# Performance work log

Measured on AMD Instinct MI355X. Metric: run time of the kernel, lower is better.

Reference implementation:

```python
import jax, jax.numpy as jnp
import numpy as np

BATCH = 16
N_ROIS = 1000
NUM_CLASSES = 81
DET_MAX = 100
MIN_CONF = 0.7
NMS_THRESH = 0.3
BBOX_STD = jnp.array([0.1, 0.1, 0.2, 0.2], jnp.float32)


def setup_inputs() -> dict:
    key = jax.random.key(0)
    k1, k2, k3, k4, k5 = jax.random.split(key, 5)
    # valid normalized boxes (y1,x1,y2,x2) with y2>y1, x2>x1
    y1 = jax.random.uniform(k1, (BATCH, N_ROIS, 1)) * 0.7
    x1 = jax.random.uniform(k2, (BATCH, N_ROIS, 1)) * 0.7
    hw = jax.random.uniform(k3, (BATCH, N_ROIS, 2)) * 0.28 + 0.02
    rois = jnp.concatenate([y1, x1, y1 + hw[..., :1], x1 + hw[..., 1:]], axis=-1)
    fpn_class = jax.nn.softmax(jax.random.normal(k4, (BATCH, N_ROIS, NUM_CLASSES)) * 2.0, axis=-1)
    fpn_bbox = jax.random.normal(k5, (BATCH, N_ROIS, NUM_CLASSES, 4)) * 0.1
    window = jnp.tile(jnp.array([[0.0, 0.0, 1.0, 1.0]], jnp.float32), (BATCH, 1))
    return {"rois": rois, "fpn_class": fpn_class, "fpn_bbox": fpn_bbox, "window": window}


def apply_box_deltas(boxes, deltas):
    # boxes [N,4] (y1,x1,y2,x2), deltas [N,4] (dy,dx,log dh,log dw)
    h = boxes[:, 2] - boxes[:, 0]
    w = boxes[:, 3] - boxes[:, 1]
    cy = boxes[:, 0] + 0.5 * h
    cx = boxes[:, 1] + 0.5 * w
    cy = cy + deltas[:, 0] * h
    cx = cx + deltas[:, 1] * w
    h = h * jnp.exp(deltas[:, 2])
    w = w * jnp.exp(deltas[:, 3])
    y1 = cy - 0.5 * h
    x1 = cx - 0.5 * w
    return jnp.stack([y1, x1, y1 + h, x1 + w], axis=1)


def clip_boxes(boxes, window):
    wy1, wx1, wy2, wx2 = window[0], window[1], window[2], window[3]
    y1 = jnp.clip(boxes[:, 0], wy1, wy2)
    x1 = jnp.clip(boxes[:, 1], wx1, wx2)
    y2 = jnp.clip(boxes[:, 2], wy1, wy2)
    x2 = jnp.clip(boxes[:, 3], wx1, wx2)
    return jnp.stack([y1, x1, y2, x2], axis=1)


def box_iou(a, b):
    # a [N,4], b [M,4] -> [N,M]
    y1 = jnp.maximum(a[:, None, 0], b[None, :, 0])
    x1 = jnp.maximum(a[:, None, 1], b[None, :, 1])
    y2 = jnp.minimum(a[:, None, 2], b[None, :, 2])
    x2 = jnp.minimum(a[:, None, 3], b[None, :, 3])
    inter = jnp.maximum(y2 - y1, 0.0) * jnp.maximum(x2 - x1, 0.0)
    area_a = (a[:, 2] - a[:, 0]) * (a[:, 3] - a[:, 1])
    area_b = (b[:, 2] - b[:, 0]) * (b[:, 3] - b[:, 1])
    union = area_a[:, None] + area_b[None, :] - inter
    return inter / jnp.maximum(union, 1e-10)


def per_class_nms_mask(boxes, class_ids, scores):
    """boxes [N,4], class_ids [N] int, scores [N] (already -1 where pre-filtered).
    Returns bool [N]: survives greedy per-class NMS (max DET_MAX kept per class)."""
    fg = jnp.arange(1, NUM_CLASSES)                       # [C-1] skip background
    sc = jnp.where(class_ids[None, :] == fg[:, None], scores[None, :], -1.0)  # [C-1,N]
    order = jnp.argsort(-sc, axis=1)                      # [C-1,N] score-desc per class
    iou = box_iou(boxes, boxes)                           # [N,N]
    col = jnp.arange(N_ROIS)
    active0 = sc >= 0.0
    kept0 = jnp.zeros_like(active0)
    cnt0 = jnp.zeros((NUM_CLASSES - 1,), jnp.int32)

    def body(i, carry):
        active, kept, cnt = carry
        cur = order[:, i]                                  # [C-1] current box idx per class
        is_act = jnp.take_along_axis(active, cur[:, None], axis=1)[:, 0]
        is_kept = is_act & (cnt < DET_MAX)
        cnt = cnt + is_kept.astype(jnp.int32)
        kept = kept | ((col[None, :] == cur[:, None]) & is_kept[:, None])
        suppress = is_kept[:, None] & (iou[cur] > NMS_THRESH)  # [C-1,N]
        active = active & ~suppress
        return (active, kept, cnt)

    _, kept, _ = jax.lax.fori_loop(0, N_ROIS, body, (active0, kept0, cnt0))
    return kept.any(axis=0)


def _refine_one(rois, probs, deltas, window):
    n = jnp.arange(N_ROIS)
    class_ids = jnp.argmax(probs, axis=1)                 # [N]
    class_scores = probs[n, class_ids]                    # [N]
    d = deltas[n, class_ids] * BBOX_STD                   # [N,4]
    refined = clip_boxes(apply_box_deltas(rois, d), window)
    keep = (class_ids > 0) & (class_scores >= MIN_CONF)
    sg = jax.lax.stop_gradient
    nms_keep = per_class_nms_mask(
        sg(refined), class_ids, jnp.where(keep, sg(class_scores), -1.0))
    keep = keep & nms_keep
    sf = jnp.where(keep, class_scores, -1.0)
    top_s, top_i = jax.lax.top_k(sf, DET_MAX)             # keep top DET_MAX overall
    valid = top_s >= 0.0
    det = jnp.concatenate(
        [refined[top_i],
         class_ids[top_i][:, None].astype(jnp.float32),
         class_scores[top_i][:, None]], axis=1)           # [DET_MAX,6]
    return jnp.where(valid[:, None], det, 0.0)            # zero-pad invalid rows


def reference(rois, fpn_class, fpn_bbox, window):
    # [B, DET_MAX, 6] = (y1,x1,y2,x2,class_id,score), normalized coords
    return jax.vmap(_refine_one)(rois, fpn_class, fpn_bbox, window)
```

## Files before the change

### kernel.cpp

```cpp
#include <hip/hip_runtime.h>
#include <math.h>

#define BATCH 16
#define N_ROIS 1000
#define NUM_CLASSES 81
#define DET_MAX 100
#define MIN_CONF 0.7f
#define NMS_THRESH 0.3f

#define ROI_TILE 128

__global__ __launch_bounds__(256) void refine_v4(
    const float* __restrict__ rois, const float* __restrict__ probs,
    const float* __restrict__ deltas, const float* __restrict__ window,
    float* __restrict__ ws_box, float* __restrict__ ws_score, int* __restrict__ ws_cls)
{
    __shared__ float s_probs[ROI_TILE * NUM_CLASSES];

    const int base_roi = blockIdx.x * ROI_TILE;

    const float4* src = (const float4*)(probs + (size_t)base_roi * NUM_CLASSES);
    float4* dst = (float4*)s_probs;
    for (int i = threadIdx.x; i < ROI_TILE * NUM_CLASSES / 4; i += 256)
        dst[i] = src[i];
    __syncthreads();

    if (threadIdx.x < ROI_TILE) {
        const int idx = base_roi + threadIdx.x;
        const int b = idx / N_ROIS;

        const float* p = s_probs + threadIdx.x * NUM_CLASSES;
        float bs0 = p[0], bs1 = p[1], bs2 = p[2], bs3 = p[3];
        int ib0 = 0, ib1 = 1, ib2 = 2, ib3 = 3;
        #pragma unroll
        for (int c = 4; c <= 76; c += 4) {
            float v0 = p[c], v1 = p[c + 1], v2 = p[c + 2], v3 = p[c + 3];
            if (v0 > bs0) { bs0 = v0; ib0 = c; }
            if (v1 > bs1) { bs1 = v1; ib1 = c + 1; }
            if (v2 > bs2) { bs2 = v2; ib2 = c + 2; }
            if (v3 > bs3) { bs3 = v3; ib3 = c + 3; }
        }
        { float v = p[80]; if (v > bs0) { bs0 = v; ib0 = 80; } }
        if (bs1 > bs0 || (bs1 == bs0 && ib1 < ib0)) { bs0 = bs1; ib0 = ib1; }
        if (bs3 > bs2 || (bs3 == bs2 && ib3 < ib2)) { bs2 = bs3; ib2 = ib3; }
        if (bs2 > bs0 || (bs2 == bs0 && ib2 < ib0)) { bs0 = bs2; ib0 = ib2; }
        const float bs = bs0;
        const int best = ib0;

        const bool keep = (best > 0) && (bs >= MIN_CONF);
        ws_score[idx] = keep ? bs : -1.0f;

        if (keep) {
            const float4 dd = ((const float4*)deltas)[(size_t)idx * NUM_CLASSES + best];
            float dy = dd.x * 0.1f, dx = dd.y * 0.1f, dh = dd.z * 0.2f, dw = dd.w * 0.2f;

            const float4 rr = ((const float4*)rois)[idx];
            float y1 = rr.x, x1 = rr.y, y2 = rr.z, x2 = rr.w;
            float h = y2 - y1, w = x2 - x1;
            float cy = y1 + 0.5f * h, cx = x1 + 0.5f * w;
            cy += dy * h;
            cx += dx * w;
            h *= expf(dh);
            w *= expf(dw);
            float ny1 = cy - 0.5f * h;
            float nx1 = cx - 0.5f * w;
            float ny2 = ny1 + h;
            float nx2 = nx1 + w;

            const float* win = window + b * 4;
            float wy1 = win[0], wx1 = win[1], wy2 = win[2], wx2 = win[3];
            ny1 = fminf(fmaxf(ny1, wy1), wy2);
            nx1 = fminf(fmaxf(nx1, wx1), wx2);
            ny2 = fminf(fmaxf(ny2, wy1), wy2);
            nx2 = fminf(fmaxf(nx2, wx1), wx2);

            ((float4*)ws_box)[idx] = make_float4(ny1, nx1, ny2, nx2);
            ws_cls[idx] = best;
        }
    }
}

__global__ __launch_bounds__(256) void nms_v4(
    const float* __restrict__ ws_box, const float* __restrict__ ws_score,
    const int* __restrict__ ws_cls, float* __restrict__ out)
{
    const int b = blockIdx.x;
    const int tid = threadIdx.x;

    __shared__ float s_cbox[N_ROIS][4];
    __shared__ float s_csc[N_ROIS];
    __shared__ short s_cidx[N_ROIS];
    __shared__ unsigned char s_ccls[N_ROIS];
    __shared__ float s_sbox[N_ROIS][4];
    __shared__ float s_ssc[N_ROIS];
    __shared__ unsigned char s_scls[N_ROIS];
    __shared__ unsigned char s_kept[N_ROIS];
    __shared__ short s_bucket[N_ROIS];
    __shared__ int s_cnt[NUM_CLASSES];
    __shared__ int s_off[NUM_CLASSES];
    __shared__ int s_C;

    if (tid == 0) s_C = 0;
    if (tid < NUM_CLASSES) s_cnt[tid] = 0;

    for (int i = tid; i < DET_MAX * 6; i += 256)
        out[(size_t)b * DET_MAX * 6 + i] = 0.0f;
    __syncthreads();

    for (int i = tid; i < N_ROIS; i += 256) {
        float sc = ws_score[b * N_ROIS + i];
        if (sc >= 0.0f) {
            int k = atomicAdd(&s_C, 1);
            s_csc[k] = sc;
            s_cidx[k] = (short)i;
            int c = ws_cls[b * N_ROIS + i];
            s_ccls[k] = (unsigned char)c;
            atomicAdd(&s_cnt[c], 1);
            float4 bb = ((const float4*)ws_box)[b * N_ROIS + i];
            s_cbox[k][0] = bb.x; s_cbox[k][1] = bb.y;
            s_cbox[k][2] = bb.z; s_cbox[k][3] = bb.w;
        }
    }
    __syncthreads();
    const int C = s_C;

    if (tid == 0) {
        int acc = 0;
        for (int c = 0; c < NUM_CLASSES; ++c) { s_off[c] = acc; acc += s_cnt[c]; }
    }
    __syncthreads();

    for (int k = tid; k < C; k += 256) {
        float sk = s_csc[k];
        int ik = s_cidx[k];
        int ck = s_ccls[k];
        int rank = 0, crank = 0;
        for (int j = 0; j < C; ++j) {
            float sj = s_csc[j];
            int before = (sj > sk) | ((sj == sk) & (s_cidx[j] < ik));
            rank += before;
            crank += before & (s_ccls[j] == ck);
        }
        s_ssc[rank] = sk;
        s_scls[rank] = (unsigned char)ck;
        s_sbox[rank][0] = s_cbox[k][0];
        s_sbox[rank][1] = s_cbox[k][1];
        s_sbox[rank][2] = s_cbox[k][2];
        s_sbox[rank][3] = s_cbox[k][3];
        s_kept[rank] = 0;
        s_bucket[s_off[ck] + crank] = (short)rank;
    }
    __syncthreads();

    if (tid >= 1 && tid < NUM_CLASSES) {
        const int off = s_off[tid];
        const int m = s_cnt[tid];
        int kept_cnt = 0;
        for (int a = 0; a < m; ++a) {
            if (kept_cnt >= DET_MAX) break;
            int i = s_bucket[off + a];
            float b0 = s_sbox[i][0], b1 = s_sbox[i][1];
            float b2 = s_sbox[i][2], b3 = s_sbox[i][3];
            float area_b = (b2 - b0) * (b3 - b1);
            bool sup = false;
            for (int q = 0; q < a; ++q) {
                int j = s_bucket[off + q];
                if (!s_kept[j]) continue;
                float a0 = s_sbox[j][0], a1 = s_sbox[j][1];
                float a2 = s_sbox[j][2], a3 = s_sbox[j][3];
                float yy1 = fmaxf(a0, b0);
                float xx1 = fmaxf(a1, b1);
                float yy2 = fminf(a2, b2);
                float xx2 = fminf(a3, b3);
                float inter = fmaxf(yy2 - yy1, 0.0f) * fmaxf(xx2 - xx1, 0.0f);
                float area_a = (a2 - a0) * (a3 - a1);
                float uni = area_a + area_b - inter;
                if (inter / fmaxf(uni, 1e-10f) > NMS_THRESH) { sup = true; break; }
            }
            if (!sup) { s_kept[i] = 1; ++kept_cnt; }
        }
    }
    __syncthreads();

    for (int i = tid; i < C; i += 256) {
        if (s_kept[i]) {
            int slot = 0;
            for (int j = 0; j < i; ++j) slot += s_kept[j];
            if (slot < DET_MAX) {
                float* o = out + (size_t)b * DET_MAX * 6 + slot * 6;
                o[0] = s_sbox[i][0];
                o[1] = s_sbox[i][1];
                o[2] = s_sbox[i][2];
                o[3] = s_sbox[i][3];
                o[4] = (float)s_scls[i];
                o[5] = s_ssc[i];
            }
        }
    }
}

extern "C" void kernel_launch(void* const* d_in, const int* in_sizes, int n_in,
                              void* d_out, int out_size, void* d_ws, size_t ws_size,
                              hipStream_t stream) {
    const float* rois      = (const float*)d_in[0];
    const float* fpn_class = (const float*)d_in[1];
    const float* fpn_bbox  = (const float*)d_in[2];
    const float* window    = (const float*)d_in[3];
    float* out = (float*)d_out;

    float* ws_box   = (float*)d_ws;
    float* ws_score = ws_box + (size_t)BATCH * N_ROIS * 4;
    int*   ws_cls   = (int*)(ws_score + (size_t)BATCH * N_ROIS);

    refine_v4<<<BATCH * N_ROIS / ROI_TILE, 256, 0, stream>>>(
        rois, fpn_class, fpn_bbox, window, ws_box, ws_score, ws_cls);
    nms_v4<<<BATCH, 256, 0, stream>>>(ws_box, ws_score, ws_cls, out);
}
```

Baseline: 85.03 us.

## Fuse refine and NMS into one per-image kernel with aliased shared memory

Merges the ROI refinement kernel into the NMS kernel so each block processes one image, tiling class probabilities through shared memory and appending kept candidates directly to shared arrays. This removes a kernel launch and the global workspace write/read between stages. Shared buffers for probs and sorted boxes are aliased, and box accesses are vectorized to float4. The refine phase now runs on only 16 blocks, which reduces parallelism for the probability scan.

```diff
diff --git a/kernel.cpp b/kernel.cpp
--- a/kernel.cpp
+++ b/kernel.cpp
@@ -8,94 +8,28 @@
 #define MIN_CONF 0.7f
 #define NMS_THRESH 0.3f
 
-#define ROI_TILE 128
+#define TILE 256
 
-__global__ __launch_bounds__(256) void refine_v4(
+__global__ __launch_bounds__(256) void detect_fused_v5(
     const float* __restrict__ rois, const float* __restrict__ probs,
     const float* __restrict__ deltas, const float* __restrict__ window,
-    float* __restrict__ ws_box, float* __restrict__ ws_score, int* __restrict__ ws_cls)
-{
-    __shared__ float s_probs[ROI_TILE * NUM_CLASSES];
-
-    const int base_roi = blockIdx.x * ROI_TILE;
-
-    const float4* src = (const float4*)(probs + (size_t)base_roi * NUM_CLASSES);
-    float4* dst = (float4*)s_probs;
-    for (int i = threadIdx.x; i < ROI_TILE * NUM_CLASSES / 4; i += 256)
-        dst[i] = src[i];
-    __syncthreads();
-
-    if (threadIdx.x < ROI_TILE) {
-        const int idx = base_roi + threadIdx.x;
-        const int b = idx / N_ROIS;
-
-        const float* p = s_probs + threadIdx.x * NUM_CLASSES;
-        float bs0 = p[0], bs1 = p[1], bs2 = p[2], bs3 = p[3];
-        int ib0 = 0, ib1 = 1, ib2 = 2, ib3 = 3;
-        #pragma unroll
-        for (int c = 4; c <= 76; c += 4) {
-            float v0 = p[c], v1 = p[c + 1], v2 = p[c + 2], v3 = p[c + 3];
-            if (v0 > bs0) { bs0 = v0; ib0 = c; }
-            if (v1 > bs1) { bs1 = v1; ib1 = c + 1; }
-            if (v2 > bs2) { bs2 = v2; ib2 = c + 2; }
-            if (v3 > bs3) { bs3 = v3; ib3 = c + 3; }
-        }
-        { float v = p[80]; if (v > bs0) { bs0 = v; ib0 = 80; } }
-        if (bs1 > bs0 || (bs1 == bs0 && ib1 < ib0)) { bs0 = bs1; ib0 = ib1; }
-        if (bs3 > bs2 || (bs3 == bs2 && ib3 < ib2)) { bs2 = bs3; ib2 = ib3; }
-        if (bs2 > bs0 || (bs2 == bs0 && ib2 < ib0)) { bs0 = bs2; ib0 = ib2; }
-        const float bs = bs0;
-        const int best = ib0;
-
-        const bool keep = (best > 0) && (bs >= MIN_CONF);
-        ws_score[idx] = keep ? bs : -1.0f;
-
-        if (keep) {
-            const float4 dd = ((const float4*)deltas)[(size_t)idx * NUM_CLASSES + best];
-            float dy = dd.x * 0.1f, dx = dd.y * 0.1f, dh = dd.z * 0.2f, dw = dd.w * 0.2f;
-
-            const float4 rr = ((const float4*)rois)[idx];
-            float y1 = rr.x, x1 = rr.y, y2 = rr.z, x2 = rr.w;
-            float h = y2 - y1, w = x2 - x1;
-            float cy = y1 + 0.5f * h, cx = x1 + 0.5f * w;
-            cy += dy * h;
-            cx += dx * w;
-            h *= expf(dh);
-            w *= expf(dw);
-            float ny1 = cy - 0.5f * h;
-            float nx1 = cx - 0.5f * w;
-            float ny2 = ny1 + h;
-            float nx2 = nx1 + w;
-
-            const float* win = window + b * 4;
-            float wy1 = win[0], wx1 = win[1], wy2 = win[2], wx2 = win[3];
-            ny1 = fminf(fmaxf(ny1, wy1), wy2);
-            nx1 = fminf(fmaxf(nx1, wx1), wx2);
-            ny2 = fminf(fmaxf(ny2, wy1), wy2);
-            nx2 = fminf(fmaxf(nx2, wx1), wx2);
-
-            ((float4*)ws_box)[idx] = make_float4(ny1, nx1, ny2, nx2);
-            ws_cls[idx] = best;
-        }
-    }
-}
-
-__global__ __launch_bounds__(256) void nms_v4(
-    const float* __restrict__ ws_box, const float* __restrict__ ws_score,
-    const int* __restrict__ ws_cls, float* __restrict__ out)
+    float* __restrict__ out)
 {
     const int b = blockIdx.x;
     const int tid = threadIdx.x;
 
-    __shared__ float s_cbox[N_ROIS][4];
+    __shared__ __align__(16) char s_raw[TILE * NUM_CLASSES * 4];
+    float* const s_probs = (float*)s_raw;
+    float (*const s_sbox)[4]    = (float(*)[4])s_raw;
+    float* const s_ssc          = (float*)(s_raw + 16000);
+    unsigned char* const s_scls = (unsigned char*)(s_raw + 20000);
+    unsigned char* const s_kept = (unsigned char*)(s_raw + 21000);
+    short* const s_bucket       = (short*)(s_raw + 22000);
+
+    __shared__ __align__(16) float s_cbox[N_ROIS][4];
     __shared__ float s_csc[N_ROIS];
     __shared__ short s_cidx[N_ROIS];
     __shared__ unsigned char s_ccls[N_ROIS];
-    __shared__ float s_sbox[N_ROIS][4];
-    __shared__ float s_ssc[N_ROIS];
-    __shared__ unsigned char s_scls[N_ROIS];
-    __shared__ unsigned char s_kept[N_ROIS];
-    __shared__ short s_bucket[N_ROIS];
     __shared__ int s_cnt[NUM_CLASSES];
     __shared__ int s_off[NUM_CLASSES];
     __shared__ int s_C;
@@ -105,23 +39,72 @@
 
     for (int i = tid; i < DET_MAX * 6; i += 256)
         out[(size_t)b * DET_MAX * 6 + i] = 0.0f;
+
+    const float4 wv = ((const float4*)window)[b];
     __syncthreads();
 
-    for (int i = tid; i < N_ROIS; i += 256) {
-        float sc = ws_score[b * N_ROIS + i];
-        if (sc >= 0.0f) {
-            int k = atomicAdd(&s_C, 1);
-            s_csc[k] = sc;
-            s_cidx[k] = (short)i;
-            int c = ws_cls[b * N_ROIS + i];
-            s_ccls[k] = (unsigned char)c;
-            atomicAdd(&s_cnt[c], 1);
-            float4 bb = ((const float4*)ws_box)[b * N_ROIS + i];
-            s_cbox[k][0] = bb.x; s_cbox[k][1] = bb.y;
-            s_cbox[k][2] = bb.z; s_cbox[k][3] = bb.w;
+    for (int t0 = 0; t0 < N_ROIS; t0 += TILE) {
+        const int tn = (N_ROIS - t0 < TILE) ? (N_ROIS - t0) : TILE;
+
+        const float4* src = (const float4*)(probs + ((size_t)b * N_ROIS + t0) * NUM_CLASSES);
+        const int n4 = tn * NUM_CLASSES / 4;
+        for (int i = tid; i < n4; i += 256)
+            ((float4*)s_probs)[i] = src[i];
+        __syncthreads();
+
+        if (tid < tn) {
+            const int r = t0 + tid;
+            const float* p = s_probs + tid * NUM_CLASSES;
+            float bs0 = p[0], bs1 = p[1], bs2 = p[2], bs3 = p[3];
+            int ib0 = 0, ib1 = 1, ib2 = 2, ib3 = 3;
+            #pragma unroll
+            for (int c = 4; c <= 76; c += 4) {
+                float v0 = p[c], v1 = p[c + 1], v2 = p[c + 2], v3 = p[c + 3];
+                if (v0 > bs0) { bs0 = v0; ib0 = c; }
+                if (v1 > bs1) { bs1 = v1; ib1 = c + 1; }
+                if (v2 > bs2) { bs2 = v2; ib2 = c + 2; }
+                if (v3 > bs3) { bs3 = v3; ib3 = c + 3; }
+            }
+            { float v = p[80]; if (v > bs0) { bs0 = v; ib0 = 80; } }
+            if (bs1 > bs0 || (bs1 == bs0 && ib1 < ib0)) { bs0 = bs1; ib0 = ib1; }
+            if (bs3 > bs2 || (bs3 == bs2 && ib3 < ib2)) { bs2 = bs3; ib2 = ib3; }
+            if (bs2 > bs0 || (bs2 == bs0 && ib2 < ib0)) { bs0 = bs2; ib0 = ib2; }
+            const float bs = bs0;
+            const int best = ib0;
+
+            if ((best > 0) && (bs >= MIN_CONF)) {
+                const size_t gidx = (size_t)b * N_ROIS + r;
+                const float4 dd = ((const float4*)deltas)[gidx * NUM_CLASSES + best];
+                float dy = dd.x * 0.1f, dx = dd.y * 0.1f, dh = dd.z * 0.2f, dw = dd.w * 0.2f;
+
+                const float4 rr = ((const float4*)rois)[gidx];
+                float y1 = rr.x, x1 = rr.y, y2 = rr.z, x2 = rr.w;
+                float h = y2 - y1, w = x2 - x1;
+                float cy = y1 + 0.5f * h, cx = x1 + 0.5f * w;
+                cy += dy * h;
+                cx += dx * w;
+                h *= expf(dh);
+                w *= expf(dw);
+                float ny1 = cy - 0.5f * h;
+                float nx1 = cx - 0.5f * w;
+                float ny2 = ny1 + h;
+                float nx2 = nx1 + w;
+
+                ny1 = fminf(fmaxf(ny1, wv.x), wv.z);
+                nx1 = fminf(fmaxf(nx1, wv.y), wv.w);
+                ny2 = fminf(fmaxf(ny2, wv.x), wv.z);
+                nx2 = fminf(fmaxf(nx2, wv.y), wv.w);
+
+                const int k = atomicAdd(&s_C, 1);
+                s_csc[k] = bs;
+                s_cidx[k] = (short)r;
+                s_ccls[k] = (unsigned char)best;
+                atomicAdd(&s_cnt[best], 1);
+                ((float4*)s_cbox)[k] = make_float4(ny1, nx1, ny2, nx2);
+            }
         }
+        __syncthreads();
     }
-    __syncthreads();
     const int C = s_C;
 
     if (tid == 0) {
@@ -143,10 +126,7 @@
         }
         s_ssc[rank] = sk;
         s_scls[rank] = (unsigned char)ck;
-        s_sbox[rank][0] = s_cbox[k][0];
-        s_sbox[rank][1] = s_cbox[k][1];
-        s_sbox[rank][2] = s_cbox[k][2];
-        s_sbox[rank][3] = s_cbox[k][3];
+        ((float4*)s_sbox)[rank] = ((const float4*)s_cbox)[k];
         s_kept[rank] = 0;
         s_bucket[s_off[ck] + crank] = (short)rank;
     }
@@ -159,21 +139,19 @@
         for (int a = 0; a < m; ++a) {
             if (kept_cnt >= DET_MAX) break;
             int i = s_bucket[off + a];
-            float b0 = s_sbox[i][0], b1 = s_sbox[i][1];
-            float b2 = s_sbox[i][2], b3 = s_sbox[i][3];
-            float area_b = (b2 - b0) * (b3 - b1);
+            float4 bb = ((const float4*)s_sbox)[i];
+            float area_b = (bb.z - bb.x) * (bb.w - bb.y);
             bool sup = false;
             for (int q = 0; q < a; ++q) {
                 int j = s_bucket[off + q];
                 if (!s_kept[j]) continue;
-                float a0 = s_sbox[j][0], a1 = s_sbox[j][1];
-                float a2 = s_sbox[j][2], a3 = s_sbox[j][3];
-                float yy1 = fmaxf(a0, b0);
-                float xx1 = fmaxf(a1, b1);
-                float yy2 = fminf(a2, b2);
-                float xx2 = fminf(a3, b3);
+                float4 aa = ((const float4*)s_sbox)[j];
+                float yy1 = fmaxf(aa.x, bb.x);
+                float xx1 = fmaxf(aa.y, bb.y);
+                float yy2 = fminf(aa.z, bb.z);
+                float xx2 = fminf(aa.w, bb.w);
                 float inter = fmaxf(yy2 - yy1, 0.0f) * fmaxf(xx2 - xx1, 0.0f);
-                float area_a = (a2 - a0) * (a3 - a1);
+                float area_a = (aa.z - aa.x) * (aa.w - aa.y);
                 float uni = area_a + area_b - inter;
                 if (inter / fmaxf(uni, 1e-10f) > NMS_THRESH) { sup = true; break; }
             }
@@ -188,10 +166,11 @@
             for (int j = 0; j < i; ++j) slot += s_kept[j];
             if (slot < DET_MAX) {
                 float* o = out + (size_t)b * DET_MAX * 6 + slot * 6;
-                o[0] = s_sbox[i][0];
-                o[1] = s_sbox[i][1];
-                o[2] = s_sbox[i][2];
-                o[3] = s_sbox[i][3];
+                float4 bb = ((const float4*)s_sbox)[i];
+                o[0] = bb.x;
+                o[1] = bb.y;
+                o[2] = bb.z;
+                o[3] = bb.w;
                 o[4] = (float)s_scls[i];
                 o[5] = s_ssc[i];
             }
@@ -207,12 +186,7 @@
     const float* fpn_bbox  = (const float*)d_in[2];
     const float* window    = (const float*)d_in[3];
     float* out = (float*)d_out;
+    (void)d_ws; (void)ws_size;
 
-    float* ws_box   = (float*)d_ws;
-    float* ws_score = ws_box + (size_t)BATCH * N_ROIS * 4;
-    int*   ws_cls   = (int*)(ws_score + (size_t)BATCH * N_ROIS);
-
-    refine_v4<<<BATCH * N_ROIS / ROI_TILE, 256, 0, stream>>>(
-        rois, fpn_class, fpn_bbox, window, ws_box, ws_score, ws_cls);
-    nms_v4<<<BATCH, 256, 0, stream>>>(ws_box, ws_score, ws_cls, out);
+    detect_fused_v5<<<BATCH, 256, 0, stream>>>(rois, fpn_class, fpn_bbox, window, out);
 }
```

Result: slower. 111.2 us (+30.8%).

## Fuse refine and NMS into one cooperative kernel with grid sync

Applied to the files above, without the earlier changes.

Merges the refine kernel and the per-batch NMS kernel into a single cooperative launch, using a grid-wide sync in place of the kernel boundary and a shared-memory arena reused by both phases. This targets the second launch's overhead and the gap between kernels. Box accesses in shared memory are also changed to float4 loads and stores. In exchange it adds a cooperative-launch and grid-barrier cost, and the larger shared footprint may limit how many blocks fit per CU.

```diff
diff --git a/kernel.cpp b/kernel.cpp
--- a/kernel.cpp
+++ b/kernel.cpp
@@ -1,5 +1,8 @@
 #include <hip/hip_runtime.h>
+#include <hip/hip_cooperative_groups.h>
 #include <math.h>
+
+namespace cg = cooperative_groups;
 
 #define BATCH 16
 #define N_ROIS 1000
@@ -9,96 +12,101 @@
 #define NMS_THRESH 0.3f
 
 #define ROI_TILE 128
-
-__global__ __launch_bounds__(256) void refine_v4(
+#define GRID_BLOCKS (BATCH * N_ROIS / ROI_TILE)
+
+__global__ __launch_bounds__(256) void detect_coop_v6(
     const float* __restrict__ rois, const float* __restrict__ probs,
     const float* __restrict__ deltas, const float* __restrict__ window,
-    float* __restrict__ ws_box, float* __restrict__ ws_score, int* __restrict__ ws_cls)
+    float* __restrict__ ws_box, float* __restrict__ ws_score,
+    int* __restrict__ ws_cls, float* __restrict__ out)
 {
-    __shared__ float s_probs[ROI_TILE * NUM_CLASSES];
-
-    const int base_roi = blockIdx.x * ROI_TILE;
-
-    const float4* src = (const float4*)(probs + (size_t)base_roi * NUM_CLASSES);
-    float4* dst = (float4*)s_probs;
-    for (int i = threadIdx.x; i < ROI_TILE * NUM_CLASSES / 4; i += 256)
-        dst[i] = src[i];
-    __syncthreads();
-
-    if (threadIdx.x < ROI_TILE) {
-        const int idx = base_roi + threadIdx.x;
-        const int b = idx / N_ROIS;
-
-        const float* p = s_probs + threadIdx.x * NUM_CLASSES;
-        float bs0 = p[0], bs1 = p[1], bs2 = p[2], bs3 = p[3];
-        int ib0 = 0, ib1 = 1, ib2 = 2, ib3 = 3;
-        #pragma unroll
-        for (int c = 4; c <= 76; c += 4) {
-            float v0 = p[c], v1 = p[c + 1], v2 = p[c + 2], v3 = p[c + 3];
-            if (v0 > bs0) { bs0 = v0; ib0 = c; }
-            if (v1 > bs1) { bs1 = v1; ib1 = c + 1; }
-            if (v2 > bs2) { bs2 = v2; ib2 = c + 2; }
-            if (v3 > bs3) { bs3 = v3; ib3 = c + 3; }
-        }
-        { float v = p[80]; if (v > bs0) { bs0 = v; ib0 = 80; } }
-        if (bs1 > bs0 || (bs1 == bs0 && ib1 < ib0)) { bs0 = bs1; ib0 = ib1; }
-        if (bs3 > bs2 || (bs3 == bs2 && ib3 < ib2)) { bs2 = bs3; ib2 = ib3; }
-        if (bs2 > bs0 || (bs2 == bs0 && ib2 < ib0)) { bs0 = bs2; ib0 = ib2; }
-        const float bs = bs0;
-        const int best = ib0;
-
-        const bool keep = (best > 0) && (bs >= MIN_CONF);
-        ws_score[idx] = keep ? bs : -1.0f;
-
-        if (keep) {
-            const float4 dd = ((const float4*)deltas)[(size_t)idx * NUM_CLASSES + best];
-            float dy = dd.x * 0.1f, dx = dd.y * 0.1f, dh = dd.z * 0.2f, dw = dd.w * 0.2f;
-
-            const float4 rr = ((const float4*)rois)[idx];
-            float y1 = rr.x, x1 = rr.y, y2 = rr.z, x2 = rr.w;
-            float h = y2 - y1, w = x2 - x1;
-            float cy = y1 + 0.5f * h, cx = x1 + 0.5f * w;
-            cy += dy * h;
-            cx += dx * w;
-            h *= expf(dh);
-            w *= expf(dw);
-            float ny1 = cy - 0.5f * h;
-            float nx1 = cx - 0.5f * w;
-            float ny2 = ny1 + h;
-            float nx2 = nx1 + w;
-
-            const float* win = window + b * 4;
-            float wy1 = win[0], wx1 = win[1], wy2 = win[2], wx2 = win[3];
-            ny1 = fminf(fmaxf(ny1, wy1), wy2);
-            nx1 = fminf(fmaxf(nx1, wx1), wx2);
-            ny2 = fminf(fmaxf(ny2, wy1), wy2);
-            nx2 = fminf(fmaxf(nx2, wx1), wx2);
-
-            ((float4*)ws_box)[idx] = make_float4(ny1, nx1, ny2, nx2);
-            ws_cls[idx] = best;
-        }
-    }
-}
-
-__global__ __launch_bounds__(256) void nms_v4(
-    const float* __restrict__ ws_box, const float* __restrict__ ws_score,
-    const int* __restrict__ ws_cls, float* __restrict__ out)
-{
-    const int b = blockIdx.x;
-    const int tid = threadIdx.x;
-
-    __shared__ float s_cbox[N_ROIS][4];
-    __shared__ float s_csc[N_ROIS];
-    __shared__ short s_cidx[N_ROIS];
-    __shared__ unsigned char s_ccls[N_ROIS];
-    __shared__ float s_sbox[N_ROIS][4];
-    __shared__ float s_ssc[N_ROIS];
-    __shared__ unsigned char s_scls[N_ROIS];
-    __shared__ unsigned char s_kept[N_ROIS];
-    __shared__ short s_bucket[N_ROIS];
+    __shared__ __align__(16) char arena[47680];
+    __shared__ int s_C;
     __shared__ int s_cnt[NUM_CLASSES];
     __shared__ int s_off[NUM_CLASSES];
-    __shared__ int s_C;
+
+    const int tid = threadIdx.x;
+
+    {
+        float* s_probs = (float*)arena;
+        const int base_roi = blockIdx.x * ROI_TILE;
+
+        const float4* src = (const float4*)(probs + (size_t)base_roi * NUM_CLASSES);
+        float4* dst = (float4*)s_probs;
+        for (int i = tid; i < ROI_TILE * NUM_CLASSES / 4; i += 256)
+            dst[i] = src[i];
+        __syncthreads();
+
+        if (tid < ROI_TILE) {
+            const int idx = base_roi + tid;
+            const int b = idx / N_ROIS;
+
+            const float* p = s_probs + tid * NUM_CLASSES;
+            float bs0 = p[0], bs1 = p[1], bs2 = p[2], bs3 = p[3];
+            int ib0 = 0, ib1 = 1, ib2 = 2, ib3 = 3;
+            #pragma unroll
+            for (int c = 4; c <= 76; c += 4) {
+                float v0 = p[c], v1 = p[c + 1], v2 = p[c + 2], v3 = p[c + 3];
+                if (v0 > bs0) { bs0 = v0; ib0 = c; }
+                if (v1 > bs1) { bs1 = v1; ib1 = c + 1; }
+                if (v2 > bs2) { bs2 = v2; ib2 = c + 2; }
+                if (v3 > bs3) { bs3 = v3; ib3 = c + 3; }
+            }
+            { float v = p[80]; if (v > bs0) { bs0 = v; ib0 = 80; } }
+            if (bs1 > bs0 || (bs1 == bs0 && ib1 < ib0)) { bs0 = bs1; ib0 = ib1; }
+            if (bs3 > bs2 || (bs3 == bs2 && ib3 < ib2)) { bs2 = bs3; ib2 = ib3; }
+            if (bs2 > bs0 || (bs2 == bs0 && ib2 < ib0)) { bs0 = bs2; ib0 = ib2; }
+            const float bs = bs0;
+            const int best = ib0;
+
+            const bool keep = (best > 0) && (bs >= MIN_CONF);
+            ws_score[idx] = keep ? bs : -1.0f;
+
+            if (keep) {
+                const float4 dd = ((const float4*)deltas)[(size_t)idx * NUM_CLASSES + best];
+                float dy = dd.x * 0.1f, dx = dd.y * 0.1f, dh = dd.z * 0.2f, dw = dd.w * 0.2f;
+
+                const float4 rr = ((const float4*)rois)[idx];
+                float y1 = rr.x, x1 = rr.y, y2 = rr.z, x2 = rr.w;
+                float h = y2 - y1, w = x2 - x1;
+                float cy = y1 + 0.5f * h, cx = x1 + 0.5f * w;
+                cy += dy * h;
+                cx += dx * w;
+                h *= expf(dh);
+                w *= expf(dw);
+                float ny1 = cy - 0.5f * h;
+                float nx1 = cx - 0.5f * w;
+                float ny2 = ny1 + h;
+                float nx2 = nx1 + w;
+
+                const float* win = window + b * 4;
+                float wy1 = win[0], wx1 = win[1], wy2 = win[2], wx2 = win[3];
+                ny1 = fminf(fmaxf(ny1, wy1), wy2);
+                nx1 = fminf(fmaxf(nx1, wx1), wx2);
+                ny2 = fminf(fmaxf(ny2, wy1), wy2);
+                nx2 = fminf(fmaxf(nx2, wx1), wx2);
+
+                ((float4*)ws_box)[idx] = make_float4(ny1, nx1, ny2, nx2);
+                ws_cls[idx] = best;
+            }
+        }
+    }
+
+    __threadfence();
+    cg::this_grid().sync();
+
+    if (blockIdx.x >= BATCH) return;
+    const int b = blockIdx.x;
+
+    float (*const s_cbox)[4]    = (float(*)[4])(arena);
+    float (*const s_sbox)[4]    = (float(*)[4])(arena + 16000);
+    float* const s_csc          = (float*)(arena + 32000);
+    float* const s_ssc          = (float*)(arena + 36000);
+    short* const s_cidx         = (short*)(arena + 40000);
+    short* const s_bucket       = (short*)(arena + 42000);
+    unsigned char* const s_ccls = (unsigned char*)(arena + 44000);
+    unsigned char* const s_scls = (unsigned char*)(arena + 45000);
+    unsigned char* const s_kept = (unsigned char*)(arena + 46000);
 
     if (tid == 0) s_C = 0;
     if (tid < NUM_CLASSES) s_cnt[tid] = 0;
@@ -117,8 +125,7 @@
             s_ccls[k] = (unsigned char)c;
             atomicAdd(&s_cnt[c], 1);
             float4 bb = ((const float4*)ws_box)[b * N_ROIS + i];
-            s_cbox[k][0] = bb.x; s_cbox[k][1] = bb.y;
-            s_cbox[k][2] = bb.z; s_cbox[k][3] = bb.w;
+            ((float4*)s_cbox)[k] = bb;
         }
     }
     __syncthreads();
@@ -143,10 +150,7 @@
         }
         s_ssc[rank] = sk;
         s_scls[rank] = (unsigned char)ck;
-        s_sbox[rank][0] = s_cbox[k][0];
-        s_sbox[rank][1] = s_cbox[k][1];
-        s_sbox[rank][2] = s_cbox[k][2];
-        s_sbox[rank][3] = s_cbox[k][3];
+        ((float4*)s_sbox)[rank] = ((const float4*)s_cbox)[k];
         s_kept[rank] = 0;
         s_bucket[s_off[ck] + crank] = (short)rank;
     }
@@ -159,21 +163,19 @@
         for (int a = 0; a < m; ++a) {
             if (kept_cnt >= DET_MAX) break;
             int i = s_bucket[off + a];
-            float b0 = s_sbox[i][0], b1 = s_sbox[i][1];
-            float b2 = s_sbox[i][2], b3 = s_sbox[i][3];
-            float area_b = (b2 - b0) * (b3 - b1);
+            float4 bb = ((const float4*)s_sbox)[i];
+            float area_b = (bb.z - bb.x) * (bb.w - bb.y);
             bool sup = false;
             for (int q = 0; q < a; ++q) {
                 int j = s_bucket[off + q];
                 if (!s_kept[j]) continue;
-                float a0 = s_sbox[j][0], a1 = s_sbox[j][1];
-                float a2 = s_sbox[j][2], a3 = s_sbox[j][3];
-                float yy1 = fmaxf(a0, b0);
-                float xx1 = fmaxf(a1, b1);
-                float yy2 = fminf(a2, b2);
-                float xx2 = fminf(a3, b3);
+                float4 aa = ((const float4*)s_sbox)[j];
+                float yy1 = fmaxf(aa.x, bb.x);
+                float xx1 = fmaxf(aa.y, bb.y);
+                float yy2 = fminf(aa.z, bb.z);
+                float xx2 = fminf(aa.w, bb.w);
                 float inter = fmaxf(yy2 - yy1, 0.0f) * fmaxf(xx2 - xx1, 0.0f);
-                float area_a = (a2 - a0) * (a3 - a1);
+                float area_a = (aa.z - aa.x) * (aa.w - aa.y);
                 float uni = area_a + area_b - inter;
                 if (inter / fmaxf(uni, 1e-10f) > NMS_THRESH) { sup = true; break; }
             }
@@ -188,10 +190,11 @@
             for (int j = 0; j < i; ++j) slot += s_kept[j];
             if (slot < DET_MAX) {
                 float* o = out + (size_t)b * DET_MAX * 6 + slot * 6;
-                o[0] = s_sbox[i][0];
-                o[1] = s_sbox[i][1];
-                o[2] = s_sbox[i][2];
-                o[3] = s_sbox[i][3];
+                float4 bb = ((const float4*)s_sbox)[i];
+                o[0] = bb.x;
+                o[1] = bb.y;
+                o[2] = bb.z;
+                o[3] = bb.w;
                 o[4] = (float)s_scls[i];
                 o[5] = s_ssc[i];
             }
@@ -212,7 +215,9 @@
     float* ws_score = ws_box + (size_t)BATCH * N_ROIS * 4;
     int*   ws_cls   = (int*)(ws_score + (size_t)BATCH * N_ROIS);
 
-    refine_v4<<<BATCH * N_ROIS / ROI_TILE, 256, 0, stream>>>(
-        rois, fpn_class, fpn_bbox, window, ws_box, ws_score, ws_cls);
-    nms_v4<<<BATCH, 256, 0, stream>>>(ws_box, ws_score, ws_cls, out);
+    void* args[] = { (void*)&rois, (void*)&fpn_class, (void*)&fpn_bbox,
+                     (void*)&window, (void*)&ws_box, (void*)&ws_score,
+                     (void*)&ws_cls, (void*)&out };
+    hipLaunchCooperativeKernel((const void*)detect_coop_v6,
+                               dim3(GRID_BLOCKS), dim3(256), args, 0, stream);
 }
```

Measured after the change: 127.6 us. 1.5x slower.

## Precompute per-class NMS suppression bitmasks in parallel before serial greedy scan

Applied to the files above, without the earlier changes.

Replaces the per-class serial NMS, where one thread per class computed IoU against earlier kept boxes, with a parallel phase in which every candidate computes a 256-bit suppression mask against later same-class boxes. A cheap serial bitmask scan per class then decides what to keep. This spreads the IoU work across all 256 threads instead of at most 80, at the cost of extra shared memory (about 32KB for the masks) and computing IoUs that the early-exit path would have skipped. Classes with more than 256 candidates fall back to the old path.

```diff
diff --git a/kernel.cpp b/kernel.cpp
--- a/kernel.cpp
+++ b/kernel.cpp
@@ -9,6 +9,7 @@
 #define NMS_THRESH 0.3f
 
 #define ROI_TILE 128
+#define SUP_WORDS 4
 
 __global__ __launch_bounds__(256) void refine_v4(
     const float* __restrict__ rois, const float* __restrict__ probs,
@@ -80,7 +81,7 @@
     }
 }
 
-__global__ __launch_bounds__(256) void nms_v4(
+__global__ __launch_bounds__(256) void nms_v5(
     const float* __restrict__ ws_box, const float* __restrict__ ws_score,
     const int* __restrict__ ws_cls, float* __restrict__ out)
 {
@@ -96,6 +97,8 @@
     __shared__ unsigned char s_scls[N_ROIS];
     __shared__ unsigned char s_kept[N_ROIS];
     __shared__ short s_bucket[N_ROIS];
+    __shared__ short s_pos[N_ROIS];
+    __shared__ unsigned long long s_sup[N_ROIS][SUP_WORDS];
     __shared__ int s_cnt[NUM_CLASSES];
     __shared__ int s_off[NUM_CLASSES];
     __shared__ int s_C;
@@ -148,26 +151,30 @@
         s_sbox[rank][2] = s_cbox[k][2];
         s_sbox[rank][3] = s_cbox[k][3];
         s_kept[rank] = 0;
+        s_pos[rank] = (short)crank;
         s_bucket[s_off[ck] + crank] = (short)rank;
     }
     __syncthreads();
 
-    if (tid >= 1 && tid < NUM_CLASSES) {
-        const int off = s_off[tid];
-        const int m = s_cnt[tid];
-        int kept_cnt = 0;
-        for (int a = 0; a < m; ++a) {
-            if (kept_cnt >= DET_MAX) break;
-            int i = s_bucket[off + a];
-            float b0 = s_sbox[i][0], b1 = s_sbox[i][1];
-            float b2 = s_sbox[i][2], b3 = s_sbox[i][3];
-            float area_b = (b2 - b0) * (b3 - b1);
-            bool sup = false;
-            for (int q = 0; q < a; ++q) {
-                int j = s_bucket[off + q];
-                if (!s_kept[j]) continue;
-                float a0 = s_sbox[j][0], a1 = s_sbox[j][1];
-                float a2 = s_sbox[j][2], a3 = s_sbox[j][3];
+    for (int u = tid; u < C; u += 256) {
+        const int i = s_bucket[u];
+        const int c = s_scls[i];
+        const int m = s_cnt[c];
+        if (m > 64 * SUP_WORDS) continue;
+        const int a = s_pos[i];
+        const int off = u - a;
+        const float b0 = s_sbox[i][0], b1 = s_sbox[i][1];
+        const float b2 = s_sbox[i][2], b3 = s_sbox[i][3];
+        const float area_b = (b2 - b0) * (b3 - b1);
+        #pragma unroll
+        for (int qw = 0; qw < SUP_WORDS; ++qw) {
+            unsigned long long w = 0;
+            const int qlo = (qw << 6) > (a + 1) ? (qw << 6) : (a + 1);
+            const int qhi = m < ((qw << 6) + 64) ? m : ((qw << 6) + 64);
+            for (int q = qlo; q < qhi; ++q) {
+                const int j = s_bucket[off + q];
+                const float a0 = s_sbox[j][0], a1 = s_sbox[j][1];
+                const float a2 = s_sbox[j][2], a3 = s_sbox[j][3];
                 float yy1 = fmaxf(a0, b0);
                 float xx1 = fmaxf(a1, b1);
                 float yy2 = fminf(a2, b2);
@@ -175,9 +182,57 @@
                 float inter = fmaxf(yy2 - yy1, 0.0f) * fmaxf(xx2 - xx1, 0.0f);
                 float area_a = (a2 - a0) * (a3 - a1);
                 float uni = area_a + area_b - inter;
-                if (inter / fmaxf(uni, 1e-10f) > NMS_THRESH) { sup = true; break; }
-            }
-            if (!sup) { s_kept[i] = 1; ++kept_cnt; }
+                w |= (unsigned long long)(inter / fmaxf(uni, 1e-10f) > NMS_THRESH)
+                     << (q & 63);
+            }
+            s_sup[u][qw] = w;
+        }
+    }
+    __syncthreads();
+
+    if (tid >= 1 && tid < NUM_CLASSES) {
+        const int off = s_off[tid];
+        const int m = s_cnt[tid];
+        if (m <= 64 * SUP_WORDS) {
+            unsigned long long r0 = 0, r1 = 0, r2 = 0, r3 = 0;
+            int cnt = 0;
+            for (int a = 0; a < m; ++a) {
+                if (cnt >= DET_MAX) break;
+                const unsigned long long rb =
+                    (a < 64) ? r0 : (a < 128) ? r1 : (a < 192) ? r2 : r3;
+                if ((rb >> (a & 63)) & 1ull) continue;
+                const int i = s_bucket[off + a];
+                s_kept[i] = 1; ++cnt;
+                r0 |= s_sup[off + a][0];
+                r1 |= s_sup[off + a][1];
+                r2 |= s_sup[off + a][2];
+                r3 |= s_sup[off + a][3];
+            }
+        } else {
+            int kept_cnt = 0;
+            for (int a = 0; a < m; ++a) {
+                if (kept_cnt >= DET_MAX) break;
+                int i = s_bucket[off + a];
+                float b0 = s_sbox[i][0], b1 = s_sbox[i][1];
+                float b2 = s_sbox[i][2], b3 = s_sbox[i][3];
+                float area_b = (b2 - b0) * (b3 - b1);
+                bool sup = false;
+                for (int q = 0; q < a; ++q) {
+                    int j = s_bucket[off + q];
+                    if (!s_kept[j]) continue;
+                    float a0 = s_sbox[j][0], a1 = s_sbox[j][1];
+                    float a2 = s_sbox[j][2], a3 = s_sbox[j][3];
+                    float yy1 = fmaxf(a0, b0);
+                    float xx1 = fmaxf(a1, b1);
+                    float yy2 = fminf(a2, b2);
+                    float xx2 = fminf(a3, b3);
+                    float inter = fmaxf(yy2 - yy1, 0.0f) * fmaxf(xx2 - xx1, 0.0f);
+                    float area_a = (a2 - a0) * (a3 - a1);
+                    float uni = area_a + area_b - inter;
+                    if (inter / fmaxf(uni, 1e-10f) > NMS_THRESH) { sup = true; break; }
+                }
+                if (!sup) { s_kept[i] = 1; ++kept_cnt; }
+            }
         }
     }
     __syncthreads();
@@ -214,5 +269,5 @@
 
     refine_v4<<<BATCH * N_ROIS / ROI_TILE, 256, 0, stream>>>(
         rois, fpn_class, fpn_bbox, window, ws_box, ws_score, ws_cls);
-    nms_v4<<<BATCH, 256, 0, stream>>>(ws_box, ws_score, ws_cls, out);
+    nms_v5<<<BATCH, 256, 0, stream>>>(ws_box, ws_score, ws_cls, out);
 }
```

New measurement: 85.72 us. No clear change (+0.8%).
